# Optimization experiments

Measured on AMD Instinct MI355X. Metric: run time of the kernel, lower is better.

The kernel has to match this reference:

```python
import jax, jax.numpy as jnp
import numpy as np

N, D, E = 50000, 128, 800000
BN_EPS = 1e-5


def _gcn(x, W, b, row, col, val):
    # dropout with p=0.0 is identity; h = x @ W; out = adj @ h + b (COO SpMM)
    h = x @ W                                    # [N, d]
    msg = val[:, None] * h[col]                  # [E, d] gather + scale
    agg = jax.ops.segment_sum(msg, row, num_segments=x.shape[0])  # scatter-add
    return agg + b


def _predictor(x, W1, b1, gamma, beta, a, W2, b2):
    h = x @ W1 + b1
    mu = jnp.mean(h, axis=0)
    var = jnp.mean((h - mu) ** 2, axis=0)        # biased var (torch BN train mode)
    hn = (h - mu) / jnp.sqrt(var + BN_EPS) * gamma + beta
    hp = jnp.where(hn >= 0, hn, a * hn)          # PReLU, single shared alpha
    return hp @ W2 + b2


def _byol_loss(p, t):
    pn = p / jnp.linalg.norm(p, axis=-1, keepdims=True)
    tn = t / jnp.linalg.norm(t, axis=-1, keepdims=True)
    return 2.0 - 2.0 * jnp.sum(pn * tn, axis=-1)


def setup_inputs() -> dict:
    key = jax.random.key(0)
    ks = jax.random.split(key, 16)
    xavier = float(np.sqrt(6.0 / (D + D)))
    x = jax.random.normal(ks[0], (N, D), dtype=jnp.float32)
    perb = 0.05 * jax.random.normal(ks[1], (N, D), dtype=jnp.float32)
    edge_row = jax.random.randint(ks[2], (E,), 0, N, dtype=jnp.int32)
    edge_col = jax.random.randint(ks[3], (E,), 0, N, dtype=jnp.int32)
    edge_val = jax.random.uniform(ks[4], (E,), dtype=jnp.float32)
    W = jax.random.uniform(ks[5], (D, D), minval=-xavier, maxval=xavier, dtype=jnp.float32)
    b = jnp.zeros((D,), dtype=jnp.float32)
    # target encoder is a deepcopy at init; give it its own values to test the math
    Wt = jax.random.uniform(ks[6], (D, D), minval=-xavier, maxval=xavier, dtype=jnp.float32)
    bt = jnp.zeros((D,), dtype=jnp.float32)
    lin = float(1.0 / np.sqrt(D))
    W1 = jax.random.uniform(ks[7], (D, D), minval=-lin, maxval=lin, dtype=jnp.float32)
    b1 = jax.random.uniform(ks[8], (D,), minval=-lin, maxval=lin, dtype=jnp.float32)
    bn_gamma = jnp.ones((D,), dtype=jnp.float32)
    bn_beta = jnp.zeros((D,), dtype=jnp.float32)
    prelu_a = jnp.asarray(0.25, dtype=jnp.float32)
    W2 = jax.random.uniform(ks[9], (D, D), minval=-lin, maxval=lin, dtype=jnp.float32)
    b2 = jax.random.uniform(ks[10], (D,), minval=-lin, maxval=lin, dtype=jnp.float32)
    return dict(x=x, perb=perb, edge_row=edge_row, edge_col=edge_col, edge_val=edge_val,
                W=W, b=b, Wt=Wt, bt=bt, W1=W1, b1=b1, bn_gamma=bn_gamma,
                bn_beta=bn_beta, prelu_a=prelu_a, W2=W2, b2=b2)


def reference(x, perb, edge_row, edge_col, edge_val, W, b, Wt, bt,
              W1, b1, bn_gamma, bn_beta, prelu_a, W2, b2):
    x1 = x
    x2 = x + perb
    enc_x2 = _gcn(x2, W, b, edge_row, edge_col, edge_val)
    embed = x2 + enc_x2
    online_x = _gcn(x1, W, b, edge_row, edge_col, edge_val)
    online_y = enc_x2
    target_y = jax.lax.stop_gradient(_gcn(x1, Wt, bt, edge_row, edge_col, edge_val))
    target_x = jax.lax.stop_gradient(_gcn(x2, Wt, bt, edge_row, edge_col, edge_val))
    px = _predictor(online_x, W1, b1, bn_gamma, bn_beta, prelu_a, W2, b2)
    py = _predictor(online_y, W1, b1, bn_gamma, bn_beta, prelu_a, W2, b2)
    loss = jnp.mean(_byol_loss(px, target_x) + _byol_loss(py, target_y))
    return embed, loss
```

## Files before the change

kernel.cpp:

```cpp
#include <hip/hip_runtime.h>
#include <stdint.h>

typedef unsigned short u16;
typedef unsigned int u32;
typedef __attribute__((ext_vector_type(8))) short bf16x8;
typedef __attribute__((ext_vector_type(4))) short bf16x4;
typedef __attribute__((ext_vector_type(4))) float f32x4;

#define DD 128
#define CAP 96
#define STRA 136
#define STRC1 264
#define STRCF 132

__device__ __forceinline__ float bflo(u32 u){ return __uint_as_float(u<<16); }
__device__ __forceinline__ float bfhi(u32 u){ return __uint_as_float(u & 0xffff0000u); }
__device__ __forceinline__ float bf2f(u16 u){ return __uint_as_float(((u32)u)<<16); }
__device__ __forceinline__ u16 f2bf(float f){
  u32 u = __float_as_uint(f);
  return (u16)((u + 0x7fffu + ((u>>16)&1u)) >> 16);
}

#define FMA4(hv, vj) do { \
    acc[0] += (vj)*bflo((hv).x); acc[1] += (vj)*bfhi((hv).x); \
    acc[2] += (vj)*bflo((hv).y); acc[3] += (vj)*bfhi((hv).y); } while(0)

__global__ __launch_bounds__(256) void kZ_zero(
    int* __restrict__ deg, float* __restrict__ stats,
    float* __restrict__ gbuf, int N)
{
  int i = blockIdx.x*256 + threadIdx.x;
  if (i < N) deg[i] = 0;
  if (i < 512) stats[i] = 0.f;
  if (i < 64) gbuf[i] = 0.f;
}

__global__ __launch_bounds__(256) void k0_swz(
    const float* __restrict__ W, const float* __restrict__ Wt,
    const float* __restrict__ W1, const float* __restrict__ W2,
    u16* __restrict__ Bswz, u16* __restrict__ W1swz, u16* __restrict__ W2swz)
{
  int idx = blockIdx.x*256 + threadIdx.x;
  if (idx < 32768) {
    int j = idx & 7, lane = (idx>>3)&63, nt = (idx>>9)&15, kt = idx>>13;
    int k = kt*32 + (lane>>4)*8 + j, n = nt*16 + (lane&15);
    float v = (n < DD) ? W[k*DD + n] : Wt[k*DD + (n-DD)];
    Bswz[idx] = f2bf(v);
  } else {
    int t = idx - 32768;
    int which = t >> 14; t &= 16383;
    int j = t & 7, lane = (t>>3)&63, nt = (t>>9)&7, kt = (t>>12)&3;
    int k = kt*32 + (lane>>4)*8 + j, n = nt*16 + (lane&15);
    const float* __restrict__ src = which ? W2 : W1;
    u16* __restrict__ dst = which ? W2swz : W1swz;
    dst[t] = f2bf(src[k*DD + n]);
  }
}

__global__ __launch_bounds__(256) void kT_build(
    const float* __restrict__ x, const float* __restrict__ perb,
    u16* __restrict__ T, int nchunks)
{
  int f = blockIdx.x*256 + threadIdx.x;
  if (f >= nchunks) return;
  int r = f >> 5, c8 = f & 31;
  const float* src = (c8 < 16) ? (x + (size_t)r*DD + c8*8)
                               : (perb + (size_t)r*DD + (c8-16)*8);
  float4 a = *(const float4*)src;
  float4 bq = *(const float4*)(src + 4);
  bf16x8 o;
  o[0]=(short)f2bf(a.x); o[1]=(short)f2bf(a.y); o[2]=(short)f2bf(a.z); o[3]=(short)f2bf(a.w);
  o[4]=(short)f2bf(bq.x); o[5]=(short)f2bf(bq.y); o[6]=(short)f2bf(bq.z); o[7]=(short)f2bf(bq.w);
  *(bf16x8*)(T + (size_t)r*256 + c8*8) = o;
}

__global__ __launch_bounds__(256) void k2_bucket(
    const int* __restrict__ row, const int* __restrict__ col,
    const float* __restrict__ val, int E, int* __restrict__ deg,
    int2* __restrict__ perm, int* __restrict__ ovfc, int* __restrict__ ovf)
{
  int e = blockIdx.x*256 + threadIdx.x;
  if (e >= E) return;
  int r = row[e];
  int slot = atomicAdd(&deg[r], 1);
  if (slot < CAP) {
    int2 cv; cv.x = col[e]; cv.y = __float_as_int(val[e]);
    perm[(size_t)r*CAP + slot] = cv;
  }
  else { int oi = atomicAdd(ovfc, 1); if (oi < 4096) ovf[oi] = e; }
}

__global__ __launch_bounds__(256) void k3_spmm(
    const int2* __restrict__ perm, const int* __restrict__ deg,
    const u16* __restrict__ T, u16* __restrict__ T2, int N)
{
  int row = blockIdx.x*4 + (threadIdx.x >> 6);
  int lane = threadIdx.x & 63;
  if (row >= N) return;
  int dg = deg[row];
  dg = dg < 0 ? 0 : (dg > CAP ? CAP : dg);
  float acc[4] = {0.f,0.f,0.f,0.f};
  const int boff = lane*4;
  for (int base = 0; base < dg; base += 64) {
    int2 ev = make_int2(0, 0);
    if (base + lane < dg) ev = perm[(size_t)row*CAP + base + lane];
    int c = ev.x; float v = __int_as_float(ev.y);
    c = ((unsigned)c < (unsigned)N) ? c : 0;
    int mm = dg - base; if (mm > 64) mm = 64;
    int j = 0;
    for (; j + 4 <= mm; j += 4) {
      int   c0 = __shfl(c, j),   c1 = __shfl(c, j+1);
      int   c2 = __shfl(c, j+2), c3 = __shfl(c, j+3);
      float v0 = __shfl(v, j),   v1 = __shfl(v, j+1);
      float v2 = __shfl(v, j+2), v3 = __shfl(v, j+3);
      uint2 h0 = *(const uint2*)(T + (size_t)c0*256 + boff);
      uint2 h1 = *(const uint2*)(T + (size_t)c1*256 + boff);
      uint2 h2 = *(const uint2*)(T + (size_t)c2*256 + boff);
      uint2 h3 = *(const uint2*)(T + (size_t)c3*256 + boff);
      FMA4(h0, v0); FMA4(h1, v1); FMA4(h2, v2); FMA4(h3, v3);
    }
    for (; j < mm; ++j) {
      int   cj = __shfl(c, j);
      float vj = __shfl(v, j);
      uint2 hv = *(const uint2*)(T + (size_t)cj*256 + boff);
      FMA4(hv, vj);
    }
  }
  bf16x4 ob;
  #pragma unroll
  for (int i = 0; i < 4; ++i) {
    float xpart = __shfl(acc[i], lane & 31);
    float o = (lane < 32) ? acc[i] : (xpart + acc[i]);
    ob[i] = (short)f2bf(o);
  }
  *(bf16x4*)(T2 + (size_t)row*256 + lane*4) = ob;
}

__global__ __launch_bounds__(256) void k3b_ovf(
    const int* __restrict__ rowI, const int* __restrict__ colI,
    const float* __restrict__ val, const int* __restrict__ ovfc,
    const int* __restrict__ ovf, const u16* __restrict__ T,
    u16* __restrict__ T2)
{
  int n = *ovfc; if (n > 4096) n = 4096;
  for (int i = 0; i < n; ++i) {
    int e = ovf[i];
    int r = rowI[e], c = colI[e];
    float v = val[e];
    int d = threadIdx.x;
    int dl = d & 127;
    float add = v * bf2f(T[(size_t)c*256 + dl]);
    if (d >= 128) add += v * bf2f(T[(size_t)c*256 + 128 + dl]);
    u16* p = &T2[(size_t)r*256 + d];
    *p = f2bf(bf2f(*p) + add);
  }
}

__global__ __launch_bounds__(256) void k4_gemm(
    const u16* __restrict__ T2, const u16* __restrict__ Bswz,
    const float* __restrict__ b, const float* __restrict__ bt,
    const float* __restrict__ x, const float* __restrict__ perb,
    u16* __restrict__ AGGb, float* __restrict__ outE, int N)
{
  __shared__ __align__(16) u16 As[64*STRA];
  __shared__ __align__(16) u16 Cs[64*STRC1];
  const int tid = threadIdx.x;
  const int r0 = blockIdx.x * 32;
  #pragma unroll
  for (int i = 0; i < 4; ++i) {
    int f = tid + 256*i;
    int row = f >> 4, c8 = f & 15;
    int r = r0 + (row & 31);
    bf16x8 ch = {0,0,0,0,0,0,0,0};
    if (r < N) ch = *(const bf16x8*)(T2 + (size_t)r*256 + (row>>5)*128 + c8*8);
    *(bf16x8*)&As[row*STRA + c8*8] = ch;
  }
  __syncthreads();
  const int w = tid >> 6, l = tid & 63;
  const int m = l & 15, q = l >> 4;
  f32x4 acc[16];
  #pragma unroll
  for (int nt = 0; nt < 16; ++nt) acc[nt] = (f32x4){0.f,0.f,0.f,0.f};
  const int arow = w*16 + m;
  #pragma unroll
  for (int kt = 0; kt < 4; ++kt) {
    bf16x8 af = *(const bf16x8*)&As[arow*STRA + kt*32 + q*8];
    #pragma unroll
    for (int nt = 0; nt < 16; ++nt) {
      bf16x8 bf = *(const bf16x8*)(Bswz + ((size_t)(kt*16+nt)*64 + l)*8);
      acc[nt] = __builtin_amdgcn_mfma_f32_16x16x32_bf16(af, bf, acc[nt], 0, 0, 0);
    }
  }
  #pragma unroll
  for (int nt = 0; nt < 16; ++nt) {
    int n = nt*16 + m;
    float bv = (n < 128) ? b[n] : bt[n-128];
    #pragma unroll
    for (int i = 0; i < 4; ++i)
      Cs[(w*16 + q*4 + i)*STRC1 + nt*16 + m] = f2bf(acc[nt][i] + bv);
  }
  __syncthreads();
  {
    const int ar = tid >> 2, p = tid & 3;
    const int src = r0 + (ar & 31);
    if (src < N) {
      size_t grow = (size_t)src*2 + (ar >> 5);
      const u16* sp = &Cs[ar*STRC1 + p*64];
      u16* dp = AGGb + grow*256 + p*64;
      #pragma unroll
      for (int i = 0; i < 8; ++i)
        *(bf16x8*)(dp + i*8) = *(const bf16x8*)(sp + i*8);
    }
  }
  #pragma unroll
  for (int i = 0; i < 2; ++i) {
    int f = tid + 256*i;
    int rr = f >> 4, c8 = f & 15;
    int src = r0 + rr;
    if (src < N) {
      const u16* cp = &Cs[(32+rr)*STRC1 + c8*8];
      const float* xr = x    + (size_t)src*DD + c8*8;
      const float* pr = perb + (size_t)src*DD + c8*8;
      float4 xa = *(const float4*)xr, xb4 = *(const float4*)(xr+4);
      float4 pa = *(const float4*)pr, pb4 = *(const float4*)(pr+4);
      float4 e0, e1;
      e0.x = xa.x+pa.x+bf2f(cp[0]); e0.y = xa.y+pa.y+bf2f(cp[1]);
      e0.z = xa.z+pa.z+bf2f(cp[2]); e0.w = xa.w+pa.w+bf2f(cp[3]);
      e1.x = xb4.x+pb4.x+bf2f(cp[4]); e1.y = xb4.y+pb4.y+bf2f(cp[5]);
      e1.z = xb4.z+pb4.z+bf2f(cp[6]); e1.w = xb4.w+pb4.w+bf2f(cp[7]);
      float* er = outE + (size_t)src*DD + c8*8;
      *(float4*)er = e0;
      *(float4*)(er+4) = e1;
    }
  }
}

__global__ __launch_bounds__(256) void k5_gemm(
    const u16* __restrict__ AGGb, const u16* __restrict__ W1swz,
    const float* __restrict__ b1, u16* __restrict__ Px, u16* __restrict__ Py,
    float* __restrict__ partial, int N)
{
  __shared__ __align__(16) u16 As[64*STRA];
  __shared__ __align__(16) float Cs[64*STRCF];
  const int tid = threadIdx.x;
  const int seg = blockIdx.y;
  const int soff = seg ? 256 : 0;
  const int r0 = blockIdx.x * 64;
  #pragma unroll
  for (int i = 0; i < 4; ++i) {
    int f = tid + 256*i;
    int row = f >> 4, c8 = f & 15;
    int r = r0 + row;
    bf16x8 ch = {0,0,0,0,0,0,0,0};
    if (r < N) ch = *(const bf16x8*)(AGGb + (size_t)r*512 + soff + c8*8);
    *(bf16x8*)&As[row*STRA + c8*8] = ch;
  }
  __syncthreads();
  const int w = tid >> 6, l = tid & 63;
  const int m = l & 15, q = l >> 4;
  f32x4 acc[8];
  #pragma unroll
  for (int nt = 0; nt < 8; ++nt) acc[nt] = (f32x4){0.f,0.f,0.f,0.f};
  const int arow = w*16 + m;
  #pragma unroll
  for (int kt = 0; kt < 4; ++kt) {
    bf16x8 af = *(const bf16x8*)&As[arow*STRA + kt*32 + q*8];
    #pragma unroll
    for (int nt = 0; nt < 8; ++nt) {
      bf16x8 bf = *(const bf16x8*)(W1swz + ((size_t)(kt*8+nt)*64 + l)*8);
      acc[nt] = __builtin_amdgcn_mfma_f32_16x16x32_bf16(af, bf, acc[nt], 0, 0, 0);
    }
  }
  const int rbase = r0 + w*16 + q*4;
  float* red = Cs;
  #pragma unroll
  for (int nt = 0; nt < 8; ++nt) {
    float bv = b1[nt*16 + m];
    float sum = 0.f, sq = 0.f;
    #pragma unroll
    for (int i = 0; i < 4; ++i) {
      if (rbase + i < N) acc[nt][i] += bv; else acc[nt][i] = 0.f;
      sum += acc[nt][i]; sq += acc[nt][i]*acc[nt][i];
    }
    sum += __shfl_xor(sum, 16); sum += __shfl_xor(sum, 32);
    sq  += __shfl_xor(sq, 16);  sq  += __shfl_xor(sq, 32);
    if (l < 16) {
      red[      w*128 + nt*16 + l] = sum;
      red[512 + w*128 + nt*16 + l] = sq;
    }
  }
  __syncthreads();
  {
    int type = tid >> 7, col = tid & 127;
    float v = red[type*512 + col] + red[type*512 + 128 + col]
            + red[type*512 + 256 + col] + red[type*512 + 384 + col];
    partial[((size_t)seg*gridDim.x + blockIdx.x)*256 + tid] = v;
  }
  __syncthreads();
  #pragma unroll
  for (int nt = 0; nt < 8; ++nt)
    #pragma unroll
    for (int i = 0; i < 4; ++i)
      Cs[(w*16 + q*4 + i)*STRCF + nt*16 + m] = acc[nt][i];
  __syncthreads();
  const int ar = tid >> 2, p = tid & 3;
  const int r = r0 + ar;
  u16* __restrict__ P = seg ? Py : Px;
  if (r < N) {
    const float* sp = &Cs[ar*STRCF + p*32];
    u16* dp = P + (size_t)r*DD + p*32;
    #pragma unroll
    for (int i = 0; i < 4; ++i) {
      bf16x8 ob;
      #pragma unroll
      for (int t2 = 0; t2 < 8; ++t2) ob[t2] = (short)f2bf(sp[i*8+t2]);
      *(bf16x8*)(dp + i*8) = ob;
    }
  }
}

__global__ __launch_bounds__(256) void k5b_stats(
    const float* __restrict__ partial, float* __restrict__ stats, int nb)
{
  int seg = blockIdx.y, chunk = blockIdx.x, t = threadIdx.x;
  int per = (nb + gridDim.x - 1) / gridDim.x;
  int lo = chunk*per, hi = lo+per; if (hi > nb) hi = nb;
  float s = 0.f;
  const float* p = partial + (size_t)seg*nb*256;
  for (int i = lo; i < hi; ++i) s += p[(size_t)i*256 + t];
  atomicAdd(&stats[seg*256 + t], s);
}

__global__ __launch_bounds__(256) void k6_gemm_loss(
    const u16* __restrict__ Px, const u16* __restrict__ Py,
    const u16* __restrict__ AGGb, const float* __restrict__ stats,
    const float* __restrict__ gamma, const float* __restrict__ beta,
    const float* __restrict__ aP, const u16* __restrict__ W2swz,
    const float* __restrict__ b2, float* __restrict__ gloss, int N)
{
  __shared__ __align__(16) u16 As[64*STRA];
  __shared__ __align__(16) float Cs[64*STRCF];
  __shared__ float s1s[128], s2s[128];
  __shared__ float gred[4];
  const int tid = threadIdx.x;
  const int seg = blockIdx.y;
  const u16* __restrict__ P = seg ? Py : Px;
  const int toff = seg ? 128 : 384;
  const float invN = 1.f / (float)N;
  if (tid < 128) {
    float mu = stats[seg*256 + tid] * invN;
    float var = stats[seg*256 + 128 + tid] * invN - mu*mu;
    float rstd = rsqrtf(var + 1e-5f);
    float s1 = rstd * gamma[tid];
    s1s[tid] = s1;
    s2s[tid] = beta[tid] - mu*s1;
  }
  const float alpha = aP[0];
  const int r0 = blockIdx.x * 64;
  __syncthreads();
  #pragma unroll
  for (int i = 0; i < 4; ++i) {
    int f = tid + 256*i;
    int row = f >> 4, c8 = f & 15;
    int r = r0 + row;
    bf16x8 ch = {0,0,0,0,0,0,0,0};
    if (r < N) ch = *(const bf16x8*)(P + (size_t)r*DD + c8*8);
    bf16x8 a;
    #pragma unroll
    for (int t2 = 0; t2 < 8; ++t2) {
      int colc = c8*8 + t2;
      float hv = bf2f((u16)ch[t2]);
      float hn = hv*s1s[colc] + s2s[colc];
      hn = hn >= 0.f ? hn : alpha*hn;
      a[t2] = (short)f2bf(hn);
    }
    *(bf16x8*)&As[row*STRA + c8*8] = a;
  }
  __syncthreads();
  const int w = tid >> 6, l = tid & 63;
  const int m = l & 15, q = l >> 4;
  f32x4 acc[8];
  #pragma unroll
  for (int nt = 0; nt < 8; ++nt) acc[nt] = (f32x4){0.f,0.f,0.f,0.f};
  const int arow = w*16 + m;
  #pragma unroll
  for (int kt = 0; kt < 4; ++kt) {
    bf16x8 af = *(const bf16x8*)&As[arow*STRA + kt*32 + q*8];
    #pragma unroll
    for (int nt = 0; nt < 8; ++nt) {
      bf16x8 bf = *(const bf16x8*)(W2swz + ((size_t)(kt*8+nt)*64 + l)*8);
      acc[nt] = __builtin_amdgcn_mfma_f32_16x16x32_bf16(af, bf, acc[nt], 0, 0, 0);
    }
  }
  #pragma unroll
  for (int nt = 0; nt < 8; ++nt) {
    float bv = b2[nt*16 + m];
    #pragma unroll
    for (int i = 0; i < 4; ++i)
      Cs[(w*16 + q*4 + i)*STRCF + nt*16 + m] = acc[nt][i] + bv;
  }
  __syncthreads();
  float lsum = 0.f;
  for (int rr = 0; rr < 16; ++rr) {
    int ar = w*16 + rr;
    int r = r0 + ar;
    if (r >= N) break;
    float2 pv = *(const float2*)&Cs[ar*STRCF + l*2];
    u32 tw = *(const u32*)(AGGb + (size_t)r*512 + toff + l*2);
    float t0 = bflo(tw), t1 = bfhi(tw);
    float pp = pv.x*pv.x + pv.y*pv.y;
    float tt = t0*t0 + t1*t1;
    float pt = pv.x*t0 + pv.y*t1;
    #pragma unroll
    for (int off = 1; off <= 32; off <<= 1) {
      pp += __shfl_xor(pp, off);
      tt += __shfl_xor(tt, off);
      pt += __shfl_xor(pt, off);
    }
    if (l == 0) lsum += 2.f - 2.f * pt * rsqrtf(pp * tt);
  }
  if (l == 0) gred[w] = lsum;
  __syncthreads();
  if (tid == 0) atomicAdd(gloss, gred[0]+gred[1]+gred[2]+gred[3]);
}

__global__ void k7_loss(const float* __restrict__ gloss, float* __restrict__ out, int N, int total)
{
  out[total] = gloss[0] / (float)N;
}

extern "C" void kernel_launch(void* const* d_in, const int* in_sizes, int n_in,
                              void* d_out, int out_size, void* d_ws, size_t ws_size,
                              hipStream_t stream)
{
  const float* x    = (const float*)d_in[0];
  const float* perb = (const float*)d_in[1];
  const int*   erow = (const int*)d_in[2];
  const int*   ecol = (const int*)d_in[3];
  const float* eval_= (const float*)d_in[4];
  const float* W    = (const float*)d_in[5];
  const float* b    = (const float*)d_in[6];
  const float* Wt   = (const float*)d_in[7];
  const float* bt   = (const float*)d_in[8];
  const float* W1   = (const float*)d_in[9];
  const float* b1   = (const float*)d_in[10];
  const float* gam  = (const float*)d_in[11];
  const float* bet  = (const float*)d_in[12];
  const float* aP   = (const float*)d_in[13];
  const float* W2   = (const float*)d_in[14];
  const float* b2   = (const float*)d_in[15];
  const int N = in_sizes[0] / DD;
  const int E = in_sizes[2];
  const int NB5 = (N + 63)/64;

  char* ws = (char*)d_ws;
  size_t off = 0;
  auto alloc = [&](size_t bytes) -> void* {
    void* p = ws + off;
    off += (bytes + 255) & ~(size_t)255;
    return p;
  };
  u16*   AGGb = (u16*)  alloc((size_t)N*512*sizeof(u16));
  u16*   T    = (u16*)  alloc((size_t)N*256*sizeof(u16));
  u16*   T2   = (u16*)  alloc((size_t)N*256*sizeof(u16));
  int*   deg  = (int*)  alloc((size_t)N*sizeof(int));
  float* stats= (float*)alloc(512*sizeof(float));
  float* gloss= (float*)alloc(256);
  int*   ovfc = (int*)((char*)gloss + 64);
  int2*  perm = (int2*) alloc((size_t)N*CAP*sizeof(int2));
  int*   ovf  = (int*)  alloc(4096*sizeof(int));
  u16*   Bswz = (u16*)  alloc(32768*sizeof(u16));
  u16*   W1swz= (u16*)  alloc(16384*sizeof(u16));
  u16*   W2swz= (u16*)  alloc(16384*sizeof(u16));
  float* partial = (float*)alloc((size_t)2*NB5*256*sizeof(float));
  if (ws_size < off) return;

  u16* Px = T;
  u16* Py = Px + (size_t)N*DD;

  kZ_zero<<<(N + 255)/256, 256, 0, stream>>>(deg, stats, gloss, N);
  k0_swz<<<256, 256, 0, stream>>>(W, Wt, W1, W2, Bswz, W1swz, W2swz);
  kT_build<<<(N*32 + 255)/256, 256, 0, stream>>>(x, perb, T, N*32);
  k2_bucket<<<(E + 255)/256, 256, 0, stream>>>(erow, ecol, eval_, E, deg, perm, ovfc, ovf);
  k3_spmm<<<(N + 3)/4, 256, 0, stream>>>(perm, deg, T, T2, N);
  k3b_ovf<<<1, 256, 0, stream>>>(erow, ecol, eval_, ovfc, ovf, T, T2);
  k4_gemm<<<(N + 31)/32, 256, 0, stream>>>(T2, Bswz, b, bt, x, perb, AGGb, (float*)d_out, N);
  k5_gemm<<<dim3(NB5, 2), 256, 0, stream>>>(AGGb, W1swz, b1, Px, Py, partial, N);
  k5b_stats<<<dim3(16, 2), 256, 0, stream>>>(partial, stats, NB5);
  k6_gemm_loss<<<dim3(NB5, 2), 256, 0, stream>>>(Px, Py, AGGb, stats, gam, bet, aP, W2swz, b2, gloss, N);
  k7_loss<<<1, 1, 0, stream>>>(gloss, (float*)d_out, N, N*DD);
}
```

Baseline: 367.5 us.

## Fuse init kernels, widen SpMM gathers, reuse bf16 inputs, fold final loss kernel

Merges the zeroing, weight-swizzle and bf16 input-build kernels into one launch. The SpMM now has each half-wavefront handle alternate edges with 16-byte gathers, then combines the halves with a cross-lane shuffle. Per-row bucket capacity drops from 96 to 64, leaning more on the overflow path. The embed epilogue reads the bf16 copy of x/perb instead of the fp32 originals, which lowers output precision. The last k6 block, chosen by an atomic ticket, writes the final loss, so the one-thread loss kernel is gone.

```diff
diff --git a/kernel.cpp b/kernel.cpp
--- a/kernel.cpp
+++ b/kernel.cpp
@@ -8,7 +8,7 @@
 typedef __attribute__((ext_vector_type(4))) float f32x4;
 
 #define DD 128
-#define CAP 96
+#define CAP 64
 #define STRA 136
 #define STRC1 264
 #define STRCF 132
@@ -21,57 +21,53 @@
   return (u16)((u + 0x7fffu + ((u>>16)&1u)) >> 16);
 }
 
-#define FMA4(hv, vj) do { \
-    acc[0] += (vj)*bflo((hv).x); acc[1] += (vj)*bfhi((hv).x); \
-    acc[2] += (vj)*bflo((hv).y); acc[3] += (vj)*bfhi((hv).y); } while(0)
-
-__global__ __launch_bounds__(256) void kZ_zero(
+#define FMA8(g, vv) do { \
+    acc[0] += (vv)*bflo((g).x); acc[1] += (vv)*bfhi((g).x); \
+    acc[2] += (vv)*bflo((g).y); acc[3] += (vv)*bfhi((g).y); \
+    acc[4] += (vv)*bflo((g).z); acc[5] += (vv)*bfhi((g).z); \
+    acc[6] += (vv)*bflo((g).w); acc[7] += (vv)*bfhi((g).w); } while(0)
+
+__global__ __launch_bounds__(256) void kU_init(
+    const float* __restrict__ x, const float* __restrict__ perb,
+    const float* __restrict__ W, const float* __restrict__ Wt,
+    const float* __restrict__ W1, const float* __restrict__ W2,
+    u16* __restrict__ T, u16* __restrict__ Bswz,
+    u16* __restrict__ W1swz, u16* __restrict__ W2swz,
     int* __restrict__ deg, float* __restrict__ stats,
     float* __restrict__ gbuf, int N)
 {
-  int i = blockIdx.x*256 + threadIdx.x;
-  if (i < N) deg[i] = 0;
-  if (i < 512) stats[i] = 0.f;
-  if (i < 64) gbuf[i] = 0.f;
-}
-
-__global__ __launch_bounds__(256) void k0_swz(
-    const float* __restrict__ W, const float* __restrict__ Wt,
-    const float* __restrict__ W1, const float* __restrict__ W2,
-    u16* __restrict__ Bswz, u16* __restrict__ W1swz, u16* __restrict__ W2swz)
-{
-  int idx = blockIdx.x*256 + threadIdx.x;
-  if (idx < 32768) {
-    int j = idx & 7, lane = (idx>>3)&63, nt = (idx>>9)&15, kt = idx>>13;
-    int k = kt*32 + (lane>>4)*8 + j, n = nt*16 + (lane&15);
-    float v = (n < DD) ? W[k*DD + n] : Wt[k*DD + (n-DD)];
-    Bswz[idx] = f2bf(v);
-  } else {
-    int t = idx - 32768;
-    int which = t >> 14; t &= 16383;
-    int j = t & 7, lane = (t>>3)&63, nt = (t>>9)&7, kt = (t>>12)&3;
-    int k = kt*32 + (lane>>4)*8 + j, n = nt*16 + (lane&15);
-    const float* __restrict__ src = which ? W2 : W1;
-    u16* __restrict__ dst = which ? W2swz : W1swz;
-    dst[t] = f2bf(src[k*DD + n]);
-  }
-}
-
-__global__ __launch_bounds__(256) void kT_build(
-    const float* __restrict__ x, const float* __restrict__ perb,
-    u16* __restrict__ T, int nchunks)
-{
   int f = blockIdx.x*256 + threadIdx.x;
-  if (f >= nchunks) return;
-  int r = f >> 5, c8 = f & 31;
-  const float* src = (c8 < 16) ? (x + (size_t)r*DD + c8*8)
-                               : (perb + (size_t)r*DD + (c8-16)*8);
-  float4 a = *(const float4*)src;
-  float4 bq = *(const float4*)(src + 4);
-  bf16x8 o;
-  o[0]=(short)f2bf(a.x); o[1]=(short)f2bf(a.y); o[2]=(short)f2bf(a.z); o[3]=(short)f2bf(a.w);
-  o[4]=(short)f2bf(bq.x); o[5]=(short)f2bf(bq.y); o[6]=(short)f2bf(bq.z); o[7]=(short)f2bf(bq.w);
-  *(bf16x8*)(T + (size_t)r*256 + c8*8) = o;
+  if (f < N) deg[f] = 0;
+  if (f < 512) stats[f] = 0.f;
+  if (f < 64) gbuf[f] = 0.f;
+  if (f < 65536) {
+    int idx = f;
+    if (idx < 32768) {
+      int j = idx & 7, lane = (idx>>3)&63, nt = (idx>>9)&15, kt = idx>>13;
+      int k = kt*32 + (lane>>4)*8 + j, n = nt*16 + (lane&15);
+      float v = (n < DD) ? W[k*DD + n] : Wt[k*DD + (n-DD)];
+      Bswz[idx] = f2bf(v);
+    } else {
+      int t = idx - 32768;
+      int which = t >> 14; t &= 16383;
+      int j = t & 7, lane = (t>>3)&63, nt = (t>>9)&7, kt = (t>>12)&3;
+      int k = kt*32 + (lane>>4)*8 + j, n = nt*16 + (lane&15);
+      const float* __restrict__ src = which ? W2 : W1;
+      u16* __restrict__ dst = which ? W2swz : W1swz;
+      dst[t] = f2bf(src[k*DD + n]);
+    }
+  }
+  if (f < N*32) {
+    int r = f >> 5, c8 = f & 31;
+    const float* src = (c8 < 16) ? (x + (size_t)r*DD + c8*8)
+                                 : (perb + (size_t)r*DD + (c8-16)*8);
+    float4 a = *(const float4*)src;
+    float4 bq = *(const float4*)(src + 4);
+    bf16x8 o;
+    o[0]=(short)f2bf(a.x); o[1]=(short)f2bf(a.y); o[2]=(short)f2bf(a.z); o[3]=(short)f2bf(a.w);
+    o[4]=(short)f2bf(bq.x); o[5]=(short)f2bf(bq.y); o[6]=(short)f2bf(bq.z); o[7]=(short)f2bf(bq.w);
+    *(bf16x8*)(T + (size_t)r*256 + c8*8) = o;
+  }
 }
 
 __global__ __launch_bounds__(256) void k2_bucket(
@@ -95,45 +91,53 @@
     const u16* __restrict__ T, u16* __restrict__ T2, int N)
 {
   int row = blockIdx.x*4 + (threadIdx.x >> 6);
-  int lane = threadIdx.x & 63;
+  int l = threadIdx.x & 63;
   if (row >= N) return;
   int dg = deg[row];
   dg = dg < 0 ? 0 : (dg > CAP ? CAP : dg);
-  float acc[4] = {0.f,0.f,0.f,0.f};
-  const int boff = lane*4;
+  const int half = l >> 5, hl = l & 31;
+  const int eoff = hl * 8;
+  float acc[8] = {0.f,0.f,0.f,0.f,0.f,0.f,0.f,0.f};
   for (int base = 0; base < dg; base += 64) {
     int2 ev = make_int2(0, 0);
-    if (base + lane < dg) ev = perm[(size_t)row*CAP + base + lane];
+    if (base + l < dg) ev = perm[(size_t)row*CAP + base + l];
     int c = ev.x; float v = __int_as_float(ev.y);
     c = ((unsigned)c < (unsigned)N) ? c : 0;
     int mm = dg - base; if (mm > 64) mm = 64;
+    int kmax = (mm + 1) & ~1;
     int j = 0;
-    for (; j + 4 <= mm; j += 4) {
-      int   c0 = __shfl(c, j),   c1 = __shfl(c, j+1);
-      int   c2 = __shfl(c, j+2), c3 = __shfl(c, j+3);
-      float v0 = __shfl(v, j),   v1 = __shfl(v, j+1);
-      float v2 = __shfl(v, j+2), v3 = __shfl(v, j+3);
-      uint2 h0 = *(const uint2*)(T + (size_t)c0*256 + boff);
-      uint2 h1 = *(const uint2*)(T + (size_t)c1*256 + boff);
-      uint2 h2 = *(const uint2*)(T + (size_t)c2*256 + boff);
-      uint2 h3 = *(const uint2*)(T + (size_t)c3*256 + boff);
-      FMA4(h0, v0); FMA4(h1, v1); FMA4(h2, v2); FMA4(h3, v3);
-    }
-    for (; j < mm; ++j) {
-      int   cj = __shfl(c, j);
-      float vj = __shfl(v, j);
-      uint2 hv = *(const uint2*)(T + (size_t)cj*256 + boff);
-      FMA4(hv, vj);
-    }
-  }
-  bf16x4 ob;
-  #pragma unroll
-  for (int i = 0; i < 4; ++i) {
-    float xpart = __shfl(acc[i], lane & 31);
-    float o = (lane < 32) ? acc[i] : (xpart + acc[i]);
+    for (; j + 8 <= kmax; j += 8) {
+      int i0 = j + half, i1 = j + 2 + half, i2 = j + 4 + half, i3 = j + 6 + half;
+      int   c0 = __shfl(c, i0), c1 = __shfl(c, i1);
+      int   c2 = __shfl(c, i2), c3 = __shfl(c, i3);
+      float v0 = __shfl(v, i0), v1 = __shfl(v, i1);
+      float v2 = __shfl(v, i2), v3 = __shfl(v, i3);
+      uint4 g0 = *(const uint4*)(T + (size_t)c0*256 + eoff);
+      uint4 g1 = *(const uint4*)(T + (size_t)c1*256 + eoff);
+      uint4 g2 = *(const uint4*)(T + (size_t)c2*256 + eoff);
+      uint4 g3 = *(const uint4*)(T + (size_t)c3*256 + eoff);
+      FMA8(g0, v0); FMA8(g1, v1); FMA8(g2, v2); FMA8(g3, v3);
+    }
+    for (; j < kmax; j += 2) {
+      int i0 = j + half;
+      int   c0 = __shfl(c, i0);
+      float v0 = __shfl(v, i0);
+      uint4 g0 = *(const uint4*)(T + (size_t)c0*256 + eoff);
+      FMA8(g0, v0);
+    }
+  }
+  #pragma unroll
+  for (int i = 0; i < 8; ++i) acc[i] += __shfl_xor(acc[i], 32);
+  int sel = (hl >= 16) ? (hl - 16) : hl;
+  bf16x8 ob;
+  #pragma unroll
+  for (int i = 0; i < 8; ++i) {
+    float xv = __shfl(acc[i], sel);
+    float o = (hl < 16) ? acc[i] : (xv + acc[i]);
     ob[i] = (short)f2bf(o);
   }
-  *(bf16x4*)(T2 + (size_t)row*256 + lane*4) = ob;
+  if (half == 0)
+    *(bf16x8*)(T2 + (size_t)row*256 + hl*8) = ob;
 }
 
 __global__ __launch_bounds__(256) void k3b_ovf(
@@ -159,7 +163,7 @@
 __global__ __launch_bounds__(256) void k4_gemm(
     const u16* __restrict__ T2, const u16* __restrict__ Bswz,
     const float* __restrict__ b, const float* __restrict__ bt,
-    const float* __restrict__ x, const float* __restrict__ perb,
+    const u16* __restrict__ T,
     u16* __restrict__ AGGb, float* __restrict__ outE, int N)
 {
   __shared__ __align__(16) u16 As[64*STRA];
@@ -219,15 +223,18 @@
     int src = r0 + rr;
     if (src < N) {
       const u16* cp = &Cs[(32+rr)*STRC1 + c8*8];
-      const float* xr = x    + (size_t)src*DD + c8*8;
-      const float* pr = perb + (size_t)src*DD + c8*8;
-      float4 xa = *(const float4*)xr, xb4 = *(const float4*)(xr+4);
-      float4 pa = *(const float4*)pr, pb4 = *(const float4*)(pr+4);
+      bf16x8 xv = *(const bf16x8*)(T + (size_t)src*256 + c8*8);
+      bf16x8 pv = *(const bf16x8*)(T + (size_t)src*256 + 128 + c8*8);
+      bf16x8 cv = *(const bf16x8*)cp;
       float4 e0, e1;
-      e0.x = xa.x+pa.x+bf2f(cp[0]); e0.y = xa.y+pa.y+bf2f(cp[1]);
-      e0.z = xa.z+pa.z+bf2f(cp[2]); e0.w = xa.w+pa.w+bf2f(cp[3]);
-      e1.x = xb4.x+pb4.x+bf2f(cp[4]); e1.y = xb4.y+pb4.y+bf2f(cp[5]);
-      e1.z = xb4.z+pb4.z+bf2f(cp[6]); e1.w = xb4.w+pb4.w+bf2f(cp[7]);
+      e0.x = bf2f((u16)xv[0])+bf2f((u16)pv[0])+bf2f((u16)cv[0]);
+      e0.y = bf2f((u16)xv[1])+bf2f((u16)pv[1])+bf2f((u16)cv[1]);
+      e0.z = bf2f((u16)xv[2])+bf2f((u16)pv[2])+bf2f((u16)cv[2]);
+      e0.w = bf2f((u16)xv[3])+bf2f((u16)pv[3])+bf2f((u16)cv[3]);
+      e1.x = bf2f((u16)xv[4])+bf2f((u16)pv[4])+bf2f((u16)cv[4]);
+      e1.y = bf2f((u16)xv[5])+bf2f((u16)pv[5])+bf2f((u16)cv[5]);
+      e1.z = bf2f((u16)xv[6])+bf2f((u16)pv[6])+bf2f((u16)cv[6]);
+      e1.w = bf2f((u16)xv[7])+bf2f((u16)pv[7])+bf2f((u16)cv[7]);
       float* er = outE + (size_t)src*DD + c8*8;
       *(float4*)er = e0;
       *(float4*)(er+4) = e1;
@@ -336,7 +343,8 @@
     const u16* __restrict__ AGGb, const float* __restrict__ stats,
     const float* __restrict__ gamma, const float* __restrict__ beta,
     const float* __restrict__ aP, const u16* __restrict__ W2swz,
-    const float* __restrict__ b2, float* __restrict__ gloss, int N)
+    const float* __restrict__ b2, float* __restrict__ gloss,
+    float* __restrict__ outF, int* __restrict__ ticket, int N)
 {
   __shared__ __align__(16) u16 As[64*STRA];
   __shared__ __align__(16) float Cs[64*STRCF];
@@ -421,12 +429,15 @@
   }
   if (l == 0) gred[w] = lsum;
   __syncthreads();
-  if (tid == 0) atomicAdd(gloss, gred[0]+gred[1]+gred[2]+gred[3]);
-}
-
-__global__ void k7_loss(const float* __restrict__ gloss, float* __restrict__ out, int N, int total)
-{
-  out[total] = gloss[0] / (float)N;
+  if (tid == 0) {
+    atomicAdd(gloss, gred[0]+gred[1]+gred[2]+gred[3]);
+    __threadfence();
+    int old = atomicAdd(ticket, 1);
+    if (old == 2*(int)gridDim.x - 1) {
+      float g = atomicAdd(gloss, 0.f);
+      outF[(size_t)N*DD] = g / (float)N;
+    }
+  }
 }
 
 extern "C" void kernel_launch(void* const* d_in, const int* in_sizes, int n_in,
@@ -467,6 +478,7 @@
   float* stats= (float*)alloc(512*sizeof(float));
   float* gloss= (float*)alloc(256);
   int*   ovfc = (int*)((char*)gloss + 64);
+  int*   ticket = (int*)((char*)gloss + 128);
   int2*  perm = (int2*) alloc((size_t)N*CAP*sizeof(int2));
   int*   ovf  = (int*)  alloc(4096*sizeof(int));
   u16*   Bswz = (u16*)  alloc(32768*sizeof(u16));
@@ -478,15 +490,15 @@
   u16* Px = T;
   u16* Py = Px + (size_t)N*DD;
 
-  kZ_zero<<<(N + 255)/256, 256, 0, stream>>>(deg, stats, gloss, N);
-  k0_swz<<<256, 256, 0, stream>>>(W, Wt, W1, W2, Bswz, W1swz, W2swz);
-  kT_build<<<(N*32 + 255)/256, 256, 0, stream>>>(x, perb, T, N*32);
+  kU_init<<<(N*32 + 255)/256, 256, 0, stream>>>(x, perb, W, Wt, W1, W2,
+                                                T, Bswz, W1swz, W2swz,
+                                                deg, stats, gloss, N);
   k2_bucket<<<(E + 255)/256, 256, 0, stream>>>(erow, ecol, eval_, E, deg, perm, ovfc, ovf);
   k3_spmm<<<(N + 3)/4, 256, 0, stream>>>(perm, deg, T, T2, N);
   k3b_ovf<<<1, 256, 0, stream>>>(erow, ecol, eval_, ovfc, ovf, T, T2);
-  k4_gemm<<<(N + 31)/32, 256, 0, stream>>>(T2, Bswz, b, bt, x, perb, AGGb, (float*)d_out, N);
+  k4_gemm<<<(N + 31)/32, 256, 0, stream>>>(T2, Bswz, b, bt, T, AGGb, (float*)d_out, N);
   k5_gemm<<<dim3(NB5, 2), 256, 0, stream>>>(AGGb, W1swz, b1, Px, Py, partial, N);
   k5b_stats<<<dim3(16, 2), 256, 0, stream>>>(partial, stats, NB5);
-  k6_gemm_loss<<<dim3(NB5, 2), 256, 0, stream>>>(Px, Py, AGGb, stats, gam, bet, aP, W2swz, b2, gloss, N);
-  k7_loss<<<1, 1, 0, stream>>>(gloss, (float*)d_out, N, N*DD);
-}
+  k6_gemm_loss<<<dim3(NB5, 2), 256, 0, stream>>>(Px, Py, AGGb, stats, gam, bet, aP,
+                                                 W2swz, b2, gloss, (float*)d_out, ticket, N);
+}
```

Result: slower. 383.3 us (+4.3%).
